# Performance work log

Hardware: AMD Instinct MI355X
Metric: run time of the kernel (lower is better)

The kernel has to match this reference:

```python
import jax, jax.numpy as jnp
import numpy as np
import math

B, T, C = 16, 1029, 1024
H, D = 16, 64  # n_heads, head_dim
NPH = NPW = 32  # 32x32 patch grid -> 1024 patch tokens
ROPE_BASE = 100.0


def _rope_cos_sin():
    # DINOv3 patch-center coordinates in [-1, 1]
    ch = (np.arange(0.5, NPH, dtype=np.float32) / NPH)
    cw = (np.arange(0.5, NPW, dtype=np.float32) / NPW)
    coords = np.stack(np.meshgrid(ch, cw, indexing='ij'), axis=-1).reshape(-1, 2)  # [N,2]
    coords = 2.0 * coords - 1.0
    inv_freq = 1.0 / ROPE_BASE ** np.arange(0, 1, 4.0 / D, dtype=np.float32)  # [D/4]
    angles = 2.0 * math.pi * coords[:, :, None] * inv_freq[None, None, :]  # [N,2,D/4]
    angles = angles.reshape(-1, D // 2)  # [N, D/2]
    angles = np.tile(angles, (1, 2))  # [N, D]
    return jnp.asarray(np.cos(angles)), jnp.asarray(np.sin(angles))


def setup_inputs() -> dict:
    key = jax.random.key(0)
    ks = jax.random.split(key, 6)
    s = 1.0 / math.sqrt(C)
    cos, sin = _rope_cos_sin()
    return {
        'x': jax.random.normal(ks[0], (B, T, C), jnp.float32),
        'Wqkv': jax.random.normal(ks[1], (C, 3 * C), jnp.float32) * s,
        'bqkv': jax.random.normal(ks[2], (3 * C,), jnp.float32) * 0.02,
        'Wout': jax.random.normal(ks[3], (C, C), jnp.float32) * s,
        'bout': jax.random.normal(ks[4], (C,), jnp.float32) * 0.02,
        'cos': cos,
        'sin': sin,
        'num_prefix': 5,  # 1 CLS + 4 registers
    }


def _rotate_half(t):
    t1, t2 = jnp.split(t, 2, axis=-1)
    return jnp.concatenate((-t2, t1), axis=-1)


def reference(x, Wqkv, bqkv, Wout, bout, cos, sin, num_prefix):
    Bx, Tx, Cx = x.shape
    qkv = x @ Wqkv + bqkv  # [B,T,3C]
    q, k, v = jnp.split(qkv, 3, axis=-1)
    to_heads = lambda t: t.reshape(Bx, Tx, H, D).transpose(0, 2, 1, 3)  # [B,H,T,D]
    q, k, v = to_heads(q), to_heads(k), to_heads(v)

    # RoPE on patch tokens only (skip CLS/register prefix)
    qp = q[:, :, num_prefix:] * cos + _rotate_half(q[:, :, num_prefix:]) * sin
    kp = k[:, :, num_prefix:] * cos + _rotate_half(k[:, :, num_prefix:]) * sin
    q = jnp.concatenate((q[:, :, :num_prefix], qp), axis=2)
    k = jnp.concatenate((k[:, :, :num_prefix], kp), axis=2)

    scale = 1.0 / math.sqrt(D)
    attn = jax.nn.softmax(jnp.einsum('bhqd,bhkd->bhqk', q, k) * scale, axis=-1)
    y = jnp.einsum('bhqk,bhkd->bhqd', attn, v)  # [B,H,T,D]
    y = y.transpose(0, 2, 1, 3).reshape(Bx, Tx, Cx)
    return y @ Wout + bout
```

## Files before the change

kernel.cpp:

```cpp
#include <hip/hip_runtime.h>
#include <hip/hip_bf16.h>
#include <stdint.h>

typedef __bf16 bf16;
typedef bf16 bf16x8 __attribute__((ext_vector_type(8)));
typedef bf16 bf16x4 __attribute__((ext_vector_type(4)));
typedef float f32x4 __attribute__((ext_vector_type(4)));

#define DEV static __device__ __forceinline__

constexpr int Bc = 16, Tc = 1029, Cc = 1024, Hc = 16, Dc = 64;
constexpr int KPAD = 1088;
constexpr int QPAD = 1152;
constexpr int MPAD = 16640;
constexpr int NKT  = KPAD / 64;
constexpr int NVT  = KPAD / 32;
constexpr int RV_SPLIT = Bc * QPAD;

DEV void gload16(void* lds_dst, const void* gsrc) {
  __builtin_amdgcn_global_load_lds(
      (const __attribute__((address_space(1))) void*)gsrc,
      (__attribute__((address_space(3))) void*)lds_dst, 16, 0, 0);
}

__global__ __launch_bounds__(256) void cast_x(const float* __restrict__ x,
                                              bf16* __restrict__ xb) {
  const size_t i = ((size_t)blockIdx.x * 256 + threadIdx.x) * 8;
  const int row = (int)(i >> 10);
  bf16x8 o = {};
  if (row < Bc * Tc) {
    const float4* p = (const float4*)(x + i);
    float4 a = p[0], b = p[1];
    o[0] = (bf16)a.x; o[1] = (bf16)a.y; o[2] = (bf16)a.z; o[3] = (bf16)a.w;
    o[4] = (bf16)b.x; o[5] = (bf16)b.y; o[6] = (bf16)b.z; o[7] = (bf16)b.w;
  }
  *(bf16x8*)(xb + i) = o;
}

__global__ __launch_bounds__(256) void transpose_cast2(const float* __restrict__ W0,
                                                       bf16* __restrict__ T0,
                                                       const float* __restrict__ W1,
                                                       bf16* __restrict__ T1) {
  const float* W; bf16* Wt; int cols;
  if (blockIdx.z == 0) { W = W0; Wt = T0; cols = 3072; }
  else { if (blockIdx.x >= 32) return; W = W1; Wt = T1; cols = 1024; }
  const int rows = 1024;
  __shared__ float tile[32][33];
  const int c0 = blockIdx.x * 32;
  const int r0 = blockIdx.y * 32;
  const int tr = threadIdx.x >> 5;
  const int tc = threadIdx.x & 31;
#pragma unroll
  for (int j = 0; j < 4; ++j)
    tile[tr + j * 8][tc] = W[(size_t)(r0 + tr + j * 8) * cols + c0 + tc];
  __syncthreads();
#pragma unroll
  for (int j = 0; j < 4; ++j)
    Wt[(size_t)(c0 + tr + j * 8) * rows + r0 + tc] = (bf16)tile[tc][tr + j * 8];
}

template <bool OUT_BF16>
__global__ __launch_bounds__(256) void gemm_bt(const bf16* __restrict__ A,
                                               const bf16* __restrict__ Bt,
                                               const float* __restrict__ bias,
                                               void* __restrict__ Cout,
                                               int N, int K, int Mlim) {
  constexpr int BM = 128, BN = 128, BK = 32;
  __shared__ bf16 As[2][BM * BK];
  __shared__ bf16 Bs[2][BN * BK];
  const int tid  = threadIdx.x;
  const int lane = tid & 63;
  const int wave = tid >> 6;
  const int g = lane >> 4;
  const int c = lane & 15;
  const int m0 = blockIdx.y * BM;
  const int n0 = blockIdx.x * BN;
  const int wm = (wave >> 1) * 64;
  const int wn = (wave & 1) * 64;

  auto stage = [&](int buf, int k0) {
#pragma unroll
    for (int j = 0; j < 2; ++j) {
      int idx = j * 256 + tid;
      int row = idx >> 2, ch = idx & 3;
      int sc = ((ch ^ ((row >> 1) & 3)) << 4);
      gload16((char*)&As[buf][0] + idx * 16,
              (const char*)(A + (size_t)(m0 + row) * K + k0) + sc);
    }
#pragma unroll
    for (int j = 0; j < 2; ++j) {
      int idx = j * 256 + tid;
      int row = idx >> 2, ch = idx & 3;
      int sc = ((ch ^ ((row >> 1) & 3)) << 4);
      gload16((char*)&Bs[buf][0] + idx * 16,
              (const char*)(Bt + (size_t)(n0 + row) * K + k0) + sc);
    }
  };

  f32x4 acc[4][4] = {};
  stage(0, 0);
  __syncthreads();
  const int nk = K / BK;
  for (int kt = 0; kt < nk; ++kt) {
    const int buf = kt & 1;
    if (kt + 1 < nk) stage(buf ^ 1, (kt + 1) * BK);
    bf16x8 af[4], bfr[4];
#pragma unroll
    for (int i = 0; i < 4; ++i) {
      const int ra = wm + i * 16 + c;
      const int rb = wn + i * 16 + c;
      af[i]  = *(const bf16x8*)((const char*)&As[buf][0] + ra * 64 +
                                (((g ^ ((ra >> 1) & 3)) << 4)));
      bfr[i] = *(const bf16x8*)((const char*)&Bs[buf][0] + rb * 64 +
                                (((g ^ ((rb >> 1) & 3)) << 4)));
    }
#pragma unroll
    for (int i = 0; i < 4; ++i)
#pragma unroll
      for (int j = 0; j < 4; ++j)
        acc[i][j] = __builtin_amdgcn_mfma_f32_16x16x32_bf16(af[i], bfr[j], acc[i][j], 0, 0, 0);
    __syncthreads();
  }

#pragma unroll
  for (int i = 0; i < 4; ++i) {
    const int mb = m0 + wm + i * 16 + g * 4;
#pragma unroll
    for (int j = 0; j < 4; ++j) {
      const int n = n0 + wn + j * 16 + c;
      const float bv = bias[n];
#pragma unroll
      for (int r = 0; r < 4; ++r) {
        const int m = mb + r;
        if (m < Mlim) {
          float v = acc[i][j][r] + bv;
          if constexpr (OUT_BF16)
            ((bf16*)Cout)[(size_t)m * N + n] = (bf16)v;
          else
            ((float*)Cout)[(size_t)m * N + n] = v;
        }
      }
    }
  }
}

__global__ __launch_bounds__(256) void rope_vtrans(const bf16* __restrict__ qkv,
                                                   const float* __restrict__ cosT,
                                                   const float* __restrict__ sinT,
                                                   const int* __restrict__ npfx_p,
                                                   bf16* __restrict__ Qh,
                                                   bf16* __restrict__ Kh,
                                                   bf16* __restrict__ Vt) {
  __shared__ bf16 lds[64][40];
  if (blockIdx.x < RV_SPLIT) {
    const int bt = blockIdx.x;
    const int b = bt / QPAD, t = bt % QPAD;
    const int h  = threadIdx.x >> 4;
    const int d0 = (threadIdx.x & 15) * 4;
    const size_t qoff = (((size_t)(b * Hc + h)) * QPAD + t) * Dc + d0;
    const size_t koff = (((size_t)(b * Hc + h)) * KPAD + t) * Dc + d0;
    if (t >= Tc) {
      bf16x4 z = {};
      *(bf16x4*)(Qh + qoff) = z;
      if (t < KPAD) *(bf16x4*)(Kh + koff) = z;
      return;
    }
    const int npfx = *npfx_p;
    const size_t inb = ((size_t)b * Tc + t) * 3072 + h * Dc;
    bf16x4 qv = *(const bf16x4*)(qkv + inb + d0);
    bf16x4 kv = *(const bf16x4*)(qkv + inb + 1024 + d0);
    float q[4], k[4];
#pragma unroll
    for (int u = 0; u < 4; ++u) { q[u] = (float)qv[u]; k[u] = (float)kv[u]; }
    if (t >= npfx) {
      const int p  = t - npfx;
      const int dp = (d0 < 32) ? d0 + 32 : d0 - 32;
      const float sgn = (d0 < 32) ? -1.f : 1.f;
      bf16x4 qp = *(const bf16x4*)(qkv + inb + dp);
      bf16x4 kp = *(const bf16x4*)(qkv + inb + 1024 + dp);
      float4 csv = *(const float4*)(cosT + (size_t)p * Dc + d0);
      float4 snv = *(const float4*)(sinT + (size_t)p * Dc + d0);
      float cs[4] = {csv.x, csv.y, csv.z, csv.w};
      float sn[4] = {snv.x, snv.y, snv.z, snv.w};
#pragma unroll
      for (int u = 0; u < 4; ++u) {
        q[u] = q[u] * cs[u] + sgn * (float)qp[u] * sn[u];
        k[u] = k[u] * cs[u] + sgn * (float)kp[u] * sn[u];
      }
    }
    bf16x4 qo, ko;
#pragma unroll
    for (int u = 0; u < 4; ++u) {
      qo[u] = (bf16)(q[u] * 0.18033688f);
      ko[u] = (bf16)k[u];
    }
    *(bf16x4*)(Qh + qoff) = qo;
    *(bf16x4*)(Kh + koff) = ko;
  } else {
    const int blk = blockIdx.x - RV_SPLIT;
    const int tt = blk % NVT;
    const int bh = blk / NVT;
    const int b = bh >> 4, h = bh & 15;
    const int t0 = tt * 32;
    const int tl = threadIdx.x >> 3;
    const int ch = threadIdx.x & 7;
    bf16x8 v = {};
    const int t = t0 + tl;
    if (t < Tc)
      v = *(const bf16x8*)(qkv + ((size_t)b * Tc + t) * 3072 + 2048 + h * Dc + ch * 8);
#pragma unroll
    for (int u = 0; u < 8; ++u) lds[ch * 8 + u][tl] = v[u];
    __syncthreads();
    const int d  = threadIdx.x >> 2;
    const int tc = threadIdx.x & 3;
    bf16x8 o = *(const bf16x8*)&lds[d][tc * 8];
    *(bf16x8*)(Vt + ((size_t)bh * Dc + d) * KPAD + t0 + tc * 8) = o;
  }
}

__global__ __launch_bounds__(256, 3) void attn4(const bf16* __restrict__ Qh,
                                                const bf16* __restrict__ Kh,
                                                const bf16* __restrict__ Vt,
                                                bf16* __restrict__ y2d) {
  __shared__ bf16 Ks[2][64 * 64];
  __shared__ bf16 Vs[2][64 * 64];
  __shared__ bf16 Ps[4][32 * 64];
  const int orig = blockIdx.x;
  const int swz = (orig & 7) * 288 + (orig >> 3);
  const int bh = swz / 9;
  const int qt = swz % 9;
  const int b = bh >> 4, h = bh & 15;
  const int tid = threadIdx.x;
  const int w = tid >> 6, lane = tid & 63;
  const int g = lane >> 4, c = lane & 15;
  const int q0 = qt * 128 + w * 32;
  const bf16* Qb = Qh + (size_t)bh * QPAD * Dc;
  const bf16* Kb = Kh + (size_t)bh * KPAD * Dc;
  const bf16* Vb = Vt + (size_t)bh * Dc * KPAD;
  char* Pw = (char*)&Ps[w][0];

  auto stage = [&](int buf, int k0) {
#pragma unroll
    for (int j = 0; j < 2; ++j) {
      int idx = j * 256 + tid;
      int row = idx >> 3;
      int scb = ((idx & 7) << 4) ^ ((row & 7) << 4);
      gload16((char*)&Ks[buf][0] + idx * 16,
              (const char*)(Kb + (size_t)(k0 + row) * 64) + scb);
    }
#pragma unroll
    for (int j = 0; j < 2; ++j) {
      int idx = j * 256 + tid;
      int row = idx >> 3;
      int scb = ((idx & 7) << 4) ^ ((row & 7) << 4);
      gload16((char*)&Vs[buf][0] + idx * 16,
              (const char*)(Vb + (size_t)row * KPAD + k0) + scb);
    }
  };

  bf16x8 qf[2][2];
#pragma unroll
  for (int fm = 0; fm < 2; ++fm)
#pragma unroll
    for (int kc = 0; kc < 2; ++kc)
      qf[fm][kc] = *(const bf16x8*)(Qb + (size_t)(q0 + fm * 16 + c) * Dc + kc * 32 + g * 8);

  bf16x8 ones;
#pragma unroll
  for (int u = 0; u < 8; ++u) ones[u] = (bf16)1.0f;

  float mrun[2] = {-1e30f, -1e30f}, lrun[2] = {0.f, 0.f};
  f32x4 oacc[2][4] = {};

  stage(0, 0);
  __syncthreads();

  for (int kt = 0; kt < NKT; ++kt) {
    const int buf = kt & 1;
    const int k0 = kt * 64;
    if (kt + 1 < NKT) stage(buf ^ 1, (kt + 1) * 64);

    f32x4 st[4][2] = {};
    __builtin_amdgcn_s_setprio(1);
#pragma unroll
    for (int fn = 0; fn < 4; ++fn) {
      const int row = fn * 16 + c;
      const int sw = (row & 7) << 4;
#pragma unroll
      for (int kc = 0; kc < 2; ++kc) {
        bf16x8 kf = *(const bf16x8*)((const char*)&Ks[buf][0] + row * 128 +
                                     ((kc * 64 + g * 16) ^ sw));
#pragma unroll
        for (int fm = 0; fm < 2; ++fm)
          st[fn][fm] = __builtin_amdgcn_mfma_f32_16x16x32_bf16(kf, qf[fm][kc], st[fn][fm], 0, 0, 0);
      }
    }
    __builtin_amdgcn_s_setprio(0);

    if (k0 + 64 > Tc) {
#pragma unroll
      for (int fn = 0; fn < 4; ++fn)
#pragma unroll
        for (int r = 0; r < 4; ++r)
          if (k0 + fn * 16 + g * 4 + r >= Tc) {
            st[fn][0][r] = -1e30f;
            st[fn][1][r] = -1e30f;
          }
    }

    float mx[2];
#pragma unroll
    for (int fm = 0; fm < 2; ++fm) {
      float m0 = fmaxf(fmaxf(st[0][fm][0], st[0][fm][1]), fmaxf(st[0][fm][2], st[0][fm][3]));
      float m1 = fmaxf(fmaxf(st[1][fm][0], st[1][fm][1]), fmaxf(st[1][fm][2], st[1][fm][3]));
      float m2 = fmaxf(fmaxf(st[2][fm][0], st[2][fm][1]), fmaxf(st[2][fm][2], st[2][fm][3]));
      float m3 = fmaxf(fmaxf(st[3][fm][0], st[3][fm][1]), fmaxf(st[3][fm][2], st[3][fm][3]));
      float m = fmaxf(fmaxf(m0, m1), fmaxf(m2, m3));
      m = fmaxf(m, __shfl_xor(m, 16));
      m = fmaxf(m, __shfl_xor(m, 32));
      mx[fm] = m;
    }
    const bool ok = (mx[0] - mrun[0] <= 11.f) && (mx[1] - mrun[1] <= 11.f);
    if (!__all(ok)) {
#pragma unroll
      for (int fm = 0; fm < 2; ++fm) {
        const float mnew = fmaxf(mrun[fm], mx[fm]);
        const float al = __builtin_amdgcn_exp2f(mrun[fm] - mnew);
        mrun[fm] = mnew;
        lrun[fm] *= al;
#pragma unroll
        for (int fd = 0; fd < 4; ++fd) oacc[fm][fd] *= al;
      }
    }
#pragma unroll
    for (int fm = 0; fm < 2; ++fm) {
      const int row = fm * 16 + c;
      const int sw = (row & 7) << 4;
#pragma unroll
      for (int fn = 0; fn < 4; ++fn) {
        bf16x4 pv;
#pragma unroll
        for (int r = 0; r < 4; ++r)
          pv[r] = (bf16)__builtin_amdgcn_exp2f(st[fn][fm][r] - mrun[fm]);
        *(bf16x4*)(Pw + row * 128 + ((fn * 32 + g * 8) ^ sw)) = pv;
      }
    }

    bf16x8 pf[2][2];
    f32x4 ps2[2] = {};
#pragma unroll
    for (int fm = 0; fm < 2; ++fm) {
      const int row = fm * 16 + c;
      const int sw = (row & 7) << 4;
#pragma unroll
      for (int kc = 0; kc < 2; ++kc) {
        pf[fm][kc] = *(const bf16x8*)(Pw + row * 128 + ((kc * 64 + g * 16) ^ sw));
        ps2[fm] = __builtin_amdgcn_mfma_f32_16x16x32_bf16(ones, pf[fm][kc], ps2[fm], 0, 0, 0);
      }
    }
    __builtin_amdgcn_s_setprio(1);
#pragma unroll
    for (int fd = 0; fd < 4; ++fd) {
      const int row = fd * 16 + c;
      const int sw = (row & 7) << 4;
#pragma unroll
      for (int kc = 0; kc < 2; ++kc) {
        bf16x8 vf = *(const bf16x8*)((const char*)&Vs[buf][0] + row * 128 +
                                     ((kc * 64 + g * 16) ^ sw));
#pragma unroll
        for (int fm = 0; fm < 2; ++fm)
          oacc[fm][fd] = __builtin_amdgcn_mfma_f32_16x16x32_bf16(vf, pf[fm][kc], oacc[fm][fd], 0, 0, 0);
      }
    }
    __builtin_amdgcn_s_setprio(0);
#pragma unroll
    for (int fm = 0; fm < 2; ++fm) lrun[fm] += ps2[fm][0];
    __syncthreads();
  }

#pragma unroll
  for (int fm = 0; fm < 2; ++fm) {
    const int trow = q0 + fm * 16 + c;
    if (trow < Tc) {
      const float inv = 1.f / lrun[fm];
#pragma unroll
      for (int fd = 0; fd < 4; ++fd) {
        bf16x4 ov;
#pragma unroll
        for (int r = 0; r < 4; ++r) ov[r] = (bf16)(oacc[fm][fd][r] * inv);
        *(bf16x4*)(y2d + ((size_t)b * Tc + trow) * Cc + h * Dc + fd * 16 + g * 4) = ov;
      }
    }
  }
}

extern "C" void kernel_launch(void* const* d_in, const int* in_sizes, int n_in,
                              void* d_out, int out_size, void* d_ws, size_t ws_size,
                              hipStream_t stream) {
  const float* x    = (const float*)d_in[0];
  const float* Wqkv = (const float*)d_in[1];
  const float* bqkv = (const float*)d_in[2];
  const float* Wout = (const float*)d_in[3];
  const float* bout = (const float*)d_in[4];
  const float* cosT = (const float*)d_in[5];
  const float* sinT = (const float*)d_in[6];
  const int*   npfx = (const int*)d_in[7];

  char* ws = (char*)d_ws;
  size_t off = 0;
  auto alloc = [&](size_t bytes) {
    char* p = ws + off;
    off = (off + bytes + 255) & ~(size_t)255;
    return p;
  };
  bf16* xb  = (bf16*)alloc((size_t)MPAD * 1024 * 2);
  bf16* Wt1 = (bf16*)alloc((size_t)3072 * 1024 * 2);
  bf16* Wt2 = (bf16*)alloc((size_t)1024 * 1024 * 2);
  bf16* qkv = (bf16*)alloc((size_t)MPAD * 3072 * 2);
  bf16* Qh  = (bf16*)alloc((size_t)256 * QPAD * 64 * 2);
  bf16* Kh  = (bf16*)alloc((size_t)256 * KPAD * 64 * 2);
  bf16* Vt  = (bf16*)alloc((size_t)256 * KPAD * 64 * 2);
  bf16* y2d = xb;
  if (off > ws_size) return;

  cast_x<<<dim3(MPAD * 1024 / 2048), dim3(256), 0, stream>>>(x, xb);
  transpose_cast2<<<dim3(96, 32, 2), dim3(256), 0, stream>>>(Wqkv, Wt1, Wout, Wt2);
  gemm_bt<true><<<dim3(3072 / 128, MPAD / 128), dim3(256), 0, stream>>>(
      xb, Wt1, bqkv, (void*)qkv, 3072, 1024, MPAD);
  rope_vtrans<<<dim3(RV_SPLIT + 256 * NVT), dim3(256), 0, stream>>>(
      qkv, cosT, sinT, npfx, Qh, Kh, Vt);
  attn4<<<dim3(2304), dim3(256), 0, stream>>>(Qh, Kh, Vt, y2d);
  gemm_bt<false><<<dim3(1024 / 128, MPAD / 128), dim3(256), 0, stream>>>(
      y2d, Wt2, bout, d_out, 1024, 1024, Bc * Tc);
}
```

Measured before the change: 382.1 us.

## Fuse RoPE and head-split scatter into QKV GEMM epilogue

The QKV projection GEMM now applies the bias, RoPE and the Q scale in its epilogue. It writes Q, K and V directly into per-head buffers, which removes the intermediate qkv tensor and the separate rope kernel pass over it. A slimmer kernel still transposes V from the new per-head layout. M padding is also reduced so fewer GEMM row tiles are launched. In exchange, the epilogue does scattered 2-byte stores and per-row cos/sin loads, and the padded Q/K rows are no longer explicitly zeroed.

```diff
diff --git a/kernel.cpp b/kernel.cpp
--- a/kernel.cpp
+++ b/kernel.cpp
@@ -12,10 +12,10 @@
 constexpr int Bc = 16, Tc = 1029, Cc = 1024, Hc = 16, Dc = 64;
 constexpr int KPAD = 1088;
 constexpr int QPAD = 1152;
-constexpr int MPAD = 16640;
+constexpr int MPAD = 16512;
+constexpr int MREAL = Bc * Tc;
 constexpr int NKT  = KPAD / 64;
 constexpr int NVT  = KPAD / 32;
-constexpr int RV_SPLIT = Bc * QPAD;
 
 DEV void gload16(void* lds_dst, const void* gsrc) {
   __builtin_amdgcn_global_load_lds(
@@ -28,7 +28,7 @@
   const size_t i = ((size_t)blockIdx.x * 256 + threadIdx.x) * 8;
   const int row = (int)(i >> 10);
   bf16x8 o = {};
-  if (row < Bc * Tc) {
+  if (row < MREAL) {
     const float4* p = (const float4*)(x + i);
     float4 a = p[0], b = p[1];
     o[0] = (bf16)a.x; o[1] = (bf16)a.y; o[2] = (bf16)a.z; o[3] = (bf16)a.w;
@@ -57,6 +57,127 @@
 #pragma unroll
   for (int j = 0; j < 4; ++j)
     Wt[(size_t)(c0 + tr + j * 8) * rows + r0 + tc] = (bf16)tile[tc][tr + j * 8];
+}
+
+__global__ __launch_bounds__(256) void gemm_qkv(const bf16* __restrict__ A,
+                                                const bf16* __restrict__ Bt,
+                                                const float* __restrict__ bias,
+                                                const float* __restrict__ cosT,
+                                                const float* __restrict__ sinT,
+                                                const int* __restrict__ npfx_p,
+                                                bf16* __restrict__ Qh,
+                                                bf16* __restrict__ Kh,
+                                                bf16* __restrict__ Vh) {
+  constexpr int BM = 128, BN = 128, BK = 32, K = 1024;
+  __shared__ bf16 As[2][BM * BK];
+  __shared__ bf16 Bs[2][BN * BK];
+  const int tid  = threadIdx.x;
+  const int lane = tid & 63;
+  const int wave = tid >> 6;
+  const int g = lane >> 4;
+  const int c = lane & 15;
+  const int m0 = blockIdx.y * BM;
+  const int n0 = blockIdx.x * BN;
+  const int wm = (wave >> 1) * 64;
+  const int wn = (wave & 1) * 64;
+
+  auto stage = [&](int buf, int k0) {
+#pragma unroll
+    for (int j = 0; j < 2; ++j) {
+      int idx = j * 256 + tid;
+      int row = idx >> 2, ch = idx & 3;
+      int sc = ((ch ^ ((row >> 1) & 3)) << 4);
+      gload16((char*)&As[buf][0] + idx * 16,
+              (const char*)(A + (size_t)(m0 + row) * K + k0) + sc);
+    }
+#pragma unroll
+    for (int j = 0; j < 2; ++j) {
+      int idx = j * 256 + tid;
+      int row = idx >> 2, ch = idx & 3;
+      int sc = ((ch ^ ((row >> 1) & 3)) << 4);
+      gload16((char*)&Bs[buf][0] + idx * 16,
+              (const char*)(Bt + (size_t)(n0 + row) * K + k0) + sc);
+    }
+  };
+
+  f32x4 acc[4][4] = {};
+  stage(0, 0);
+  __syncthreads();
+  const int nk = K / BK;
+  for (int kt = 0; kt < nk; ++kt) {
+    const int buf = kt & 1;
+    if (kt + 1 < nk) stage(buf ^ 1, (kt + 1) * BK);
+    bf16x8 af[4], bfr[4];
+#pragma unroll
+    for (int i = 0; i < 4; ++i) {
+      const int ra = wm + i * 16 + c;
+      const int rb = wn + i * 16 + c;
+      af[i]  = *(const bf16x8*)((const char*)&As[buf][0] + ra * 64 +
+                                (((g ^ ((ra >> 1) & 3)) << 4)));
+      bfr[i] = *(const bf16x8*)((const char*)&Bs[buf][0] + rb * 64 +
+                                (((g ^ ((rb >> 1) & 3)) << 4)));
+    }
+#pragma unroll
+    for (int i = 0; i < 4; ++i)
+#pragma unroll
+      for (int j = 0; j < 4; ++j)
+        acc[i][j] = __builtin_amdgcn_mfma_f32_16x16x32_bf16(af[i], bfr[j], acc[i][j], 0, 0, 0);
+    __syncthreads();
+  }
+
+  const int npfx = *npfx_p;
+  const int n_base = n0 + wn;
+  const int region = n_base >> 10;
+  const int h = (n_base & 1023) >> 6;
+  float bv[4];
+#pragma unroll
+  for (int j = 0; j < 4; ++j) bv[j] = bias[n_base + j * 16 + c];
+
+#pragma unroll
+  for (int i = 0; i < 4; ++i) {
+    const int mb = m0 + wm + i * 16 + g * 4;
+#pragma unroll
+    for (int r = 0; r < 4; ++r) {
+      const int m = mb + r;
+      if (m >= MREAL) continue;
+      const int b = m / Tc;
+      const int t = m - b * Tc;
+      float val[4];
+#pragma unroll
+      for (int j = 0; j < 4; ++j) val[j] = acc[i][j][r] + bv[j];
+      const int bh = b * Hc + h;
+      if (region == 2) {
+        bf16* dst = Vh + (((size_t)bh * Tc + t) * 64);
+#pragma unroll
+        for (int j = 0; j < 4; ++j) dst[j * 16 + c] = (bf16)val[j];
+      } else {
+        float out[4];
+        if (t >= npfx) {
+          const int p = t - npfx;
+#pragma unroll
+          for (int j = 0; j < 4; ++j) {
+            const float cs = cosT[p * 64 + j * 16 + c];
+            const float sn = sinT[p * 64 + j * 16 + c];
+            const float sgn = (j < 2) ? -1.f : 1.f;
+            out[j] = val[j] * cs + sgn * val[j ^ 2] * sn;
+          }
+        } else {
+#pragma unroll
+          for (int j = 0; j < 4; ++j) out[j] = val[j];
+        }
+        if (region == 0) {
+          bf16* dst = Qh + (((size_t)bh * QPAD + t) * 64);
+#pragma unroll
+          for (int j = 0; j < 4; ++j)
+            dst[j * 16 + c] = (bf16)(out[j] * 0.18033688f);
+        } else {
+          bf16* dst = Kh + (((size_t)bh * KPAD + t) * 64);
+#pragma unroll
+          for (int j = 0; j < 4; ++j) dst[j * 16 + c] = (bf16)out[j];
+        }
+      }
+    }
+  }
 }
 
 template <bool OUT_BF16>
@@ -144,78 +265,26 @@
   }
 }
 
-__global__ __launch_bounds__(256) void rope_vtrans(const bf16* __restrict__ qkv,
-                                                   const float* __restrict__ cosT,
-                                                   const float* __restrict__ sinT,
-                                                   const int* __restrict__ npfx_p,
-                                                   bf16* __restrict__ Qh,
-                                                   bf16* __restrict__ Kh,
-                                                   bf16* __restrict__ Vt) {
+__global__ __launch_bounds__(256) void vtrans2(const bf16* __restrict__ Vh,
+                                               bf16* __restrict__ Vt) {
   __shared__ bf16 lds[64][40];
-  if (blockIdx.x < RV_SPLIT) {
-    const int bt = blockIdx.x;
-    const int b = bt / QPAD, t = bt % QPAD;
-    const int h  = threadIdx.x >> 4;
-    const int d0 = (threadIdx.x & 15) * 4;
-    const size_t qoff = (((size_t)(b * Hc + h)) * QPAD + t) * Dc + d0;
-    const size_t koff = (((size_t)(b * Hc + h)) * KPAD + t) * Dc + d0;
-    if (t >= Tc) {
-      bf16x4 z = {};
-      *(bf16x4*)(Qh + qoff) = z;
-      if (t < KPAD) *(bf16x4*)(Kh + koff) = z;
-      return;
-    }
-    const int npfx = *npfx_p;
-    const size_t inb = ((size_t)b * Tc + t) * 3072 + h * Dc;
-    bf16x4 qv = *(const bf16x4*)(qkv + inb + d0);
-    bf16x4 kv = *(const bf16x4*)(qkv + inb + 1024 + d0);
-    float q[4], k[4];
-#pragma unroll
-    for (int u = 0; u < 4; ++u) { q[u] = (float)qv[u]; k[u] = (float)kv[u]; }
-    if (t >= npfx) {
-      const int p  = t - npfx;
-      const int dp = (d0 < 32) ? d0 + 32 : d0 - 32;
-      const float sgn = (d0 < 32) ? -1.f : 1.f;
-      bf16x4 qp = *(const bf16x4*)(qkv + inb + dp);
-      bf16x4 kp = *(const bf16x4*)(qkv + inb + 1024 + dp);
-      float4 csv = *(const float4*)(cosT + (size_t)p * Dc + d0);
-      float4 snv = *(const float4*)(sinT + (size_t)p * Dc + d0);
-      float cs[4] = {csv.x, csv.y, csv.z, csv.w};
-      float sn[4] = {snv.x, snv.y, snv.z, snv.w};
-#pragma unroll
-      for (int u = 0; u < 4; ++u) {
-        q[u] = q[u] * cs[u] + sgn * (float)qp[u] * sn[u];
-        k[u] = k[u] * cs[u] + sgn * (float)kp[u] * sn[u];
-      }
-    }
-    bf16x4 qo, ko;
-#pragma unroll
-    for (int u = 0; u < 4; ++u) {
-      qo[u] = (bf16)(q[u] * 0.18033688f);
-      ko[u] = (bf16)k[u];
-    }
-    *(bf16x4*)(Qh + qoff) = qo;
-    *(bf16x4*)(Kh + koff) = ko;
-  } else {
-    const int blk = blockIdx.x - RV_SPLIT;
-    const int tt = blk % NVT;
-    const int bh = blk / NVT;
-    const int b = bh >> 4, h = bh & 15;
-    const int t0 = tt * 32;
-    const int tl = threadIdx.x >> 3;
-    const int ch = threadIdx.x & 7;
-    bf16x8 v = {};
-    const int t = t0 + tl;
-    if (t < Tc)
-      v = *(const bf16x8*)(qkv + ((size_t)b * Tc + t) * 3072 + 2048 + h * Dc + ch * 8);
-#pragma unroll
-    for (int u = 0; u < 8; ++u) lds[ch * 8 + u][tl] = v[u];
-    __syncthreads();
-    const int d  = threadIdx.x >> 2;
-    const int tc = threadIdx.x & 3;
-    bf16x8 o = *(const bf16x8*)&lds[d][tc * 8];
-    *(bf16x8*)(Vt + ((size_t)bh * Dc + d) * KPAD + t0 + tc * 8) = o;
-  }
+  const int blk = blockIdx.x;
+  const int tt = blk % NVT;
+  const int bh = blk / NVT;
+  const int t0 = tt * 32;
+  const int tl = threadIdx.x >> 3;
+  const int ch = threadIdx.x & 7;
+  bf16x8 v = {};
+  const int t = t0 + tl;
+  if (t < Tc)
+    v = *(const bf16x8*)(Vh + ((size_t)bh * Tc + t) * 64 + ch * 8);
+#pragma unroll
+  for (int u = 0; u < 8; ++u) lds[ch * 8 + u][tl] = v[u];
+  __syncthreads();
+  const int d  = threadIdx.x >> 2;
+  const int tc = threadIdx.x & 3;
+  bf16x8 o = *(const bf16x8*)&lds[d][tc * 8];
+  *(bf16x8*)(Vt + ((size_t)bh * Dc + d) * KPAD + t0 + tc * 8) = o;
 }
 
 __global__ __launch_bounds__(256, 3) void attn4(const bf16* __restrict__ Qh,
@@ -416,20 +485,19 @@
   bf16* xb  = (bf16*)alloc((size_t)MPAD * 1024 * 2);
   bf16* Wt1 = (bf16*)alloc((size_t)3072 * 1024 * 2);
   bf16* Wt2 = (bf16*)alloc((size_t)1024 * 1024 * 2);
-  bf16* qkv = (bf16*)alloc((size_t)MPAD * 3072 * 2);
   bf16* Qh  = (bf16*)alloc((size_t)256 * QPAD * 64 * 2);
   bf16* Kh  = (bf16*)alloc((size_t)256 * KPAD * 64 * 2);
+  bf16* Vh  = (bf16*)alloc((size_t)256 * Tc * 64 * 2);
   bf16* Vt  = (bf16*)alloc((size_t)256 * KPAD * 64 * 2);
   bf16* y2d = xb;
   if (off > ws_size) return;
 
   cast_x<<<dim3(MPAD * 1024 / 2048), dim3(256), 0, stream>>>(x, xb);
   transpose_cast2<<<dim3(96, 32, 2), dim3(256), 0, stream>>>(Wqkv, Wt1, Wout, Wt2);
-  gemm_bt<true><<<dim3(3072 / 128, MPAD / 128), dim3(256), 0, stream>>>(
-      xb, Wt1, bqkv, (void*)qkv, 3072, 1024, MPAD);
-  rope_vtrans<<<dim3(RV_SPLIT + 256 * NVT), dim3(256), 0, stream>>>(
-      qkv, cosT, sinT, npfx, Qh, Kh, Vt);
+  gemm_qkv<<<dim3(3072 / 128, MPAD / 128), dim3(256), 0, stream>>>(
+      xb, Wt1, bqkv, cosT, sinT, npfx, Qh, Kh, Vh);
+  vtrans2<<<dim3(256 * NVT), dim3(256), 0, stream>>>(Vh, Vt);
   attn4<<<dim3(2304), dim3(256), 0, stream>>>(Qh, Kh, Vt, y2d);
   gemm_bt<false><<<dim3(1024 / 128, MPAD / 128), dim3(256), 0, stream>>>(
-      y2d, Wt2, bout, d_out, 1024, 1024, Bc * Tc);
-}
+      y2d, Wt2, bout, d_out, 1024, 1024, MREAL);
+}
```

New measurement: 374.6 us. About the same (-2.0%).
